# Kernel optimization log

Measured on AMD Instinct MI355X. Metric: run time of the kernel, lower is better.

Reference implementation:

```python
import jax, jax.numpy as jnp
import numpy as np
from jax import lax

VOC = 32000; H = 512; T = 256; B = 64; L = 2; MAXLEN = 32; SOS = 1


def setup_inputs() -> dict:
    key = jax.random.key(0)
    ks = jax.random.split(key, 20)
    s = 1.0 / np.sqrt(H)
    u = lambda k, shape: jax.random.uniform(k, shape, jnp.float32, -s, s)
    inp = {}
    inp["input"] = jax.random.randint(ks[0], (T, B), 0, VOC)
    inp["emb_enc"] = jax.random.normal(ks[1], (VOC, H), jnp.float32) * 0.1
    inp["emb_dec"] = jax.random.normal(ks[2], (VOC, H), jnp.float32) * 0.1
    # GRU weights, torch layout: W_ih (3H, in), W_hh (3H, H), biases (3H,); stacked over layers
    inp["enc_Wih"] = u(ks[3], (L, 3 * H, H)); inp["enc_Whh"] = u(ks[4], (L, 3 * H, H))
    inp["enc_bih"] = u(ks[5], (L, 3 * H));   inp["enc_bhh"] = u(ks[6], (L, 3 * H))
    inp["dec_Wih"] = u(ks[7], (L, 3 * H, H)); inp["dec_Whh"] = u(ks[8], (L, 3 * H, H))
    inp["dec_bih"] = u(ks[9], (L, 3 * H));   inp["dec_bhh"] = u(ks[10], (L, 3 * H))
    inp["attn_W"] = u(ks[11], (T, (L + 1) * H)); inp["attn_b"] = u(ks[12], (T,))
    inp["comb_W"] = u(ks[13], (H, 2 * H));       inp["comb_b"] = u(ks[14], (H,))
    inp["avg_W"] = u(ks[15], (1, H))   # dueling value head, no bias
    inp["adv_W"] = u(ks[16], (VOC, H)) # dueling advantage head, no bias
    return inp


def _gru_cell(x, h, Wih, Whh, bih, bhh):
    gi = x @ Wih.T + bih
    gh = h @ Whh.T + bhh
    ir, iz, in_ = jnp.split(gi, 3, axis=-1)
    hr, hz, hn = jnp.split(gh, 3, axis=-1)
    r = jax.nn.sigmoid(ir + hr)
    z = jax.nn.sigmoid(iz + hz)
    n = jnp.tanh(in_ + r * hn)
    return (1.0 - z) * n + z * h


def _gru_step(x, h, Wih, Whh, bih, bhh):
    # x: (B,H), h: (L,B,H) -> new h (L,B,H), top-layer output (B,H)
    hs = []
    for l in range(L):
        hl = _gru_cell(x, h[l], Wih[l], Whh[l], bih[l], bhh[l])
        hs.append(hl)
        x = hl
    return jnp.stack(hs), x


def _forward(input, emb_enc, emb_dec, enc_Wih, enc_Whh, enc_bih, enc_bhh,
             dec_Wih, dec_Whh, dec_bih, dec_bhh, attn_W, attn_b,
             comb_W, comb_b, avg_W, adv_W):
    # ----- encoder -----
    emb = jax.nn.relu(emb_enc[input])  # (T,B,H)
    h0 = jnp.zeros((L, B, H), jnp.float32)

    def enc_step(h, x):
        h2, top = _gru_step(x, h, enc_Wih, enc_Whh, enc_bih, enc_bhh)
        return h2, top

    states, gru_out = lax.scan(enc_step, h0, emb)  # gru_out: (T,B,H)

    def dec_step(carry, _):
        h, word = carry
        e = jax.nn.relu(emb_dec[word])                       # (B,H)
        sv = jnp.reshape(h, (B, L * H))                      # matches torch .view(-1,1,L*H)
        a = jax.nn.relu(jnp.concatenate([e, sv], -1) @ attn_W.T + attn_b)  # (B,T)
        applied = jnp.einsum('bt,tbh->bh', a, gru_out)       # (B,H)
        comb = jax.nn.relu(jnp.concatenate([e, applied], -1) @ comb_W.T + comb_b)
        h2, top = _gru_step(comb, h, dec_Wih, dec_Whh, dec_bih, dec_bhh)
        values = top @ avg_W.T + top @ adv_W.T               # (B,1)+(B,VOC) -> (B,VOC)
        word2 = jnp.argmax(values, axis=-1)
        q = jnp.take_along_axis(values, word2[:, None], axis=-1)[:, 0]
        return (h2, word2), (top, q)

    word0 = jnp.full((B,), SOS, dtype=jnp.int32)
    _, (tops, qs) = lax.scan(dec_step, (states, word0), None, length=MAXLEN)
    sentences = tops[:, None]  # (MAXLEN,1,B,H) mirrors stacking (1,B,H) rnn_outs
    return sentences, qs       # qs: (MAXLEN,B)


def reference(input, emb_enc, emb_dec, enc_Wih, enc_Whh, enc_bih, enc_bhh,
              dec_Wih, dec_Whh, dec_bih, dec_bhh, attn_W, attn_b,
              comb_W, comb_b, avg_W, adv_W):
    return _forward(input, emb_enc, emb_dec, enc_Wih, enc_Whh, enc_bih, enc_bhh,
                    dec_Wih, dec_Whh, dec_bih, dec_bhh, attn_W, attn_b,
                    comb_W, comb_b, avg_W, adv_W)
```

## Files before the change

### kernel.cpp

```cpp
#include <hip/hip_runtime.h>
#include <math.h>

#define VOCN 32000
#define HN 512
#define TN 256
#define BN 64
#define MAXLENN 32
#define SOSW 1

#define WS_FLAG     0
#define WS_REL      8192
#define WS_H        8448
#define WS_CELLS    (WS_H + 131072)
#define WS_AVG      (WS_CELLS + 4096)
#define WS_A        (WS_AVG + 64)
#define WS_APPLIED  (WS_A + 16384)
#define WS_COMB     (WS_APPLIED + 32768)
#define WS_GRUOUT   (WS_COMB + 32768)
#define WS_ZERO_BYTES ((WS_CELLS + 4096) * 4)

typedef float f4 __attribute__((ext_vector_type(4)));

__device__ __forceinline__ f4 ld4(const float* p) { return *(const f4*)p; }
__device__ __forceinline__ f4 ldnt4(const float* p) {
  return __builtin_nontemporal_load((const f4*)p);
}
__device__ __forceinline__ float dot4(f4 a, f4 b, float acc) {
  acc = fmaf(a.x, b.x, acc); acc = fmaf(a.y, b.y, acc);
  acc = fmaf(a.z, b.z, acc); acc = fmaf(a.w, b.w, acc); return acc;
}
__device__ __forceinline__ f4 relu4(f4 v) {
  v.x = fmaxf(v.x, 0.f); v.y = fmaxf(v.y, 0.f);
  v.z = fmaxf(v.z, 0.f); v.w = fmaxf(v.w, 0.f); return v;
}
__device__ __forceinline__ float sigmoidf_(float x) { return 1.f / (1.f + expf(-x)); }

__device__ __forceinline__ float ldcg(const float* p) {
  float v;
  asm volatile("global_load_dword %0, %1, off sc0 sc1\n\ts_waitcnt vmcnt(0)"
               : "=&v"(v) : "v"(p) : "memory");
  return v;
}
__device__ __forceinline__ void stcg(float* p, float v) {
  asm volatile("global_store_dword %0, %1, off sc0 sc1" :: "v"(p), "v"(v) : "memory");
}
__device__ __forceinline__ void ldcg_b4(const float* p0, const float* p1,
                                        const float* p2, const float* p3,
                                        f4& v0, f4& v1, f4& v2, f4& v3) {
  asm volatile(
      "global_load_dwordx4 %0, %4, off sc0 sc1\n\t"
      "global_load_dwordx4 %1, %5, off sc0 sc1\n\t"
      "global_load_dwordx4 %2, %6, off sc0 sc1\n\t"
      "global_load_dwordx4 %3, %7, off sc0 sc1\n\t"
      "s_waitcnt vmcnt(0)"
      : "=&v"(v0), "=&v"(v1), "=&v"(v2), "=&v"(v3)
      : "v"(p0), "v"(p1), "v"(p2), "v"(p3)
      : "memory");
}
__device__ __forceinline__ void ldcg_b8(const float* p0, const float* p1,
    const float* p2, const float* p3, const float* p4, const float* p5,
    const float* p6, const float* p7,
    f4& v0, f4& v1, f4& v2, f4& v3, f4& v4, f4& v5, f4& v6, f4& v7) {
  asm volatile(
      "global_load_dwordx4 %0, %8, off sc0 sc1\n\t"
      "global_load_dwordx4 %1, %9, off sc0 sc1\n\t"
      "global_load_dwordx4 %2, %10, off sc0 sc1\n\t"
      "global_load_dwordx4 %3, %11, off sc0 sc1\n\t"
      "global_load_dwordx4 %4, %12, off sc0 sc1\n\t"
      "global_load_dwordx4 %5, %13, off sc0 sc1\n\t"
      "global_load_dwordx4 %6, %14, off sc0 sc1\n\t"
      "global_load_dwordx4 %7, %15, off sc0 sc1\n\t"
      "s_waitcnt vmcnt(0)"
      : "=&v"(v0), "=&v"(v1), "=&v"(v2), "=&v"(v3),
        "=&v"(v4), "=&v"(v5), "=&v"(v6), "=&v"(v7)
      : "v"(p0), "v"(p1), "v"(p2), "v"(p3), "v"(p4), "v"(p5), "v"(p6), "v"(p7)
      : "memory");
}
__device__ __forceinline__ void ldcg_row8(const float* p, f4 (&v)[8]) {
  asm volatile(
      "global_load_dwordx4 %0, %8, off sc0 sc1\n\t"
      "global_load_dwordx4 %1, %8, off offset:16 sc0 sc1\n\t"
      "global_load_dwordx4 %2, %8, off offset:32 sc0 sc1\n\t"
      "global_load_dwordx4 %3, %8, off offset:48 sc0 sc1\n\t"
      "global_load_dwordx4 %4, %8, off offset:64 sc0 sc1\n\t"
      "global_load_dwordx4 %5, %8, off offset:80 sc0 sc1\n\t"
      "global_load_dwordx4 %6, %8, off offset:96 sc0 sc1\n\t"
      "global_load_dwordx4 %7, %8, off offset:112 sc0 sc1\n\t"
      "s_waitcnt vmcnt(0)"
      : "=&v"(v[0]), "=&v"(v[1]), "=&v"(v[2]), "=&v"(v[3]),
        "=&v"(v[4]), "=&v"(v[5]), "=&v"(v[6]), "=&v"(v[7])
      : "v"(p)
      : "memory");
}

__device__ __forceinline__ void grid_barrier(int* wsi, int gen) {
  asm volatile("s_waitcnt vmcnt(0) lgkmcnt(0)" ::: "memory");
  __syncthreads();
  const int bid = blockIdx.x;
  const int tid = threadIdx.x;
  if (bid == 0) {
    if (tid == 0)
      __hip_atomic_store(wsi + WS_FLAG, gen, __ATOMIC_RELAXED, __HIP_MEMORY_SCOPE_AGENT);
    int* fp = wsi + WS_FLAG + (tid & 255) * 32;
    for (;;) {
      int v = gen;
      if (tid < 256)
        v = __hip_atomic_load(fp, __ATOMIC_RELAXED, __HIP_MEMORY_SCOPE_AGENT);
      if (__syncthreads_and(v >= gen)) break;
      __builtin_amdgcn_s_sleep(2);
    }
    if (tid < 8)
      __hip_atomic_store(wsi + WS_REL + tid * 16, gen, __ATOMIC_RELAXED, __HIP_MEMORY_SCOPE_AGENT);
    __syncthreads();
  } else {
    if (tid == 0) {
      __hip_atomic_store(wsi + WS_FLAG + bid * 32, gen, __ATOMIC_RELAXED, __HIP_MEMORY_SCOPE_AGENT);
      int* rp = wsi + WS_REL + (bid & 7) * 16;
      while (__hip_atomic_load(rp, __ATOMIC_RELAXED, __HIP_MEMORY_SCOPE_AGENT) < gen)
        __builtin_amdgcn_s_sleep(2);
    }
    __syncthreads();
  }
}

__device__ __forceinline__ unsigned ord_enc(float v) {
  unsigned u = __float_as_uint(v);
  return (u & 0x80000000u) ? ~u : (u | 0x80000000u);
}
__device__ __forceinline__ float ord_dec(unsigned k32) {
  unsigned u = (k32 & 0x80000000u) ? (k32 ^ 0x80000000u) : ~k32;
  return __uint_as_float(u);
}
__device__ __forceinline__ int decode_word(const unsigned long long* cell) {
  unsigned long long key = __hip_atomic_load(cell, __ATOMIC_RELAXED,
                                             __HIP_MEMORY_SCOPE_AGENT);
  int wb = (int)(0xFFFFFFFFu - (unsigned)(key & 0xFFFFFFFFull));
  return wb < 0 ? 0 : (wb > VOCN - 1 ? VOCN - 1 : wb);
}

__device__ __forceinline__ void gru_phase(
    const float* __restrict__ x_base, const int* __restrict__ tok,
    const float* __restrict__ h_rows,
    const float* __restrict__ Wih, const float* __restrict__ Whh,
    const float* __restrict__ bih, const float* __restrict__ bhh,
    float* __restrict__ h_out, float* __restrict__ aux_out,
    int jg, float* lds)
{
  const int tid = threadIdx.x;
  const int tid2 = tid & 255;
  const int bg = tid >> 8;
  f4* x4l = (f4*)lds + (bg << 11);
  f4* h4l = x4l + 1024;

  const float* xp[4]; const float* hp[4]; int loff[4];
#pragma unroll
  for (int i = 0; i < 4; ++i) {
    int tau = tid2 + (i << 8);
    int b = tau >> 5;
    int kq = tau & 31;
    int gb = bg * 32 + b;
    const float* xr = tok ? (x_base + (size_t)tok[gb] * HN) : (x_base + (size_t)gb * HN);
    xp[i] = xr + (kq << 2);
    hp[i] = h_rows + (size_t)gb * HN + (kq << 2);
    loff[i] = (b << 5) + (kq ^ (b & 7));
  }
  const bool cachedx = (tok != nullptr);
  f4 pxv[4], phv[4];
  if (cachedx) {
#pragma unroll
    for (int i = 0; i < 4; ++i) pxv[i] = ld4(xp[i]);
    ldcg_b4(hp[0], hp[1], hp[2], hp[3], phv[0], phv[1], phv[2], phv[3]);
  } else {
    ldcg_b8(xp[0], xp[1], xp[2], xp[3], hp[0], hp[1], hp[2], hp[3],
            pxv[0], pxv[1], pxv[2], pxv[3], phv[0], phv[1], phv[2], phv[3]);
  }

  const int bl = tid2 & 31;
  const int jl = tid2 >> 5;
  const int j = (jg << 3) + jl;
  const float* wi0 = Wih + (size_t)j * HN;
  const float* wi1 = Wih + (size_t)(512 + j) * HN;
  const float* wi2 = Wih + (size_t)(1024 + j) * HN;
  const float* wh0 = Whh + (size_t)j * HN;
  const float* wh1 = Whh + (size_t)(512 + j) * HN;
  const float* wh2 = Whh + (size_t)(1024 + j) * HN;
  float ax0 = 0.f, ax1 = 0.f, ax2 = 0.f, ah0 = 0.f, ah1 = 0.f, ah2 = 0.f;
  const int rdbase = bl << 5;
  const int rdx = bl & 7;

#pragma unroll 1
  for (int ch = 0; ch < 4; ++ch) {
    __syncthreads();
#pragma unroll
    for (int i = 0; i < 4; ++i) {
      x4l[loff[i]] = cachedx ? relu4(pxv[i]) : pxv[i];
      h4l[loff[i]] = phv[i];
    }
    __syncthreads();
    if (ch < 3) {
      const int off = (ch + 1) * 128;
      if (cachedx) {
#pragma unroll
        for (int i = 0; i < 4; ++i) pxv[i] = ld4(xp[i] + off);
        ldcg_b4(hp[0] + off, hp[1] + off, hp[2] + off, hp[3] + off,
                phv[0], phv[1], phv[2], phv[3]);
      } else {
        ldcg_b8(xp[0] + off, xp[1] + off, xp[2] + off, xp[3] + off,
                hp[0] + off, hp[1] + off, hp[2] + off, hp[3] + off,
                pxv[0], pxv[1], pxv[2], pxv[3], phv[0], phv[1], phv[2], phv[3]);
      }
    }
    const int k0 = ch << 7;
#pragma unroll 4
    for (int kq = 0; kq < 32; ++kq) {
      f4 xv = x4l[rdbase + (kq ^ rdx)];
      f4 hv = h4l[rdbase + (kq ^ rdx)];
      const int kk = k0 + (kq << 2);
      ax0 = dot4(xv, ld4(wi0 + kk), ax0);
      ah0 = dot4(hv, ld4(wh0 + kk), ah0);
      ax1 = dot4(xv, ld4(wi1 + kk), ax1);
      ah1 = dot4(hv, ld4(wh1 + kk), ah1);
      ax2 = dot4(xv, ld4(wi2 + kk), ax2);
      ah2 = dot4(hv, ld4(wh2 + kk), ah2);
    }
  }
  const int gb = bg * 32 + bl;
  const float hold = ldcg(h_rows + (size_t)gb * HN + j);
  const float r = sigmoidf_(ax0 + bih[j] + ah0 + bhh[j]);
  const float z = sigmoidf_(ax1 + bih[512 + j] + ah1 + bhh[512 + j]);
  const float n = tanhf(ax2 + bih[1024 + j] + r * (ah2 + bhh[1024 + j]));
  const float hv = (1.f - z) * n + z * hold;
  stcg(h_out + (size_t)gb * HN + j, hv);
  if (aux_out) stcg(aux_out + (size_t)gb * HN + j, hv);
}

__device__ __forceinline__ void d1_attn(
    const float* __restrict__ emb_dec, const unsigned long long* __restrict__ cells,
    int s, const float* __restrict__ hflat, const float* __restrict__ attn_W,
    const float* __restrict__ attn_b, float* __restrict__ a_buf,
    const float* __restrict__ avg_buf, float* __restrict__ qs_base,
    int bid, float* lds)
{
  const int tid = threadIdx.x;
  const int b = tid & 63, q = tid >> 6;
  int* wlds = (int*)(lds + 576);
  if (s > 0 && tid < 64)
    wlds[tid] = decode_word(cells + (size_t)(s - 1) * 64 + tid);
  if (s > 0 && bid == 0 && tid < 64) {
    unsigned long long key = __hip_atomic_load(cells + (size_t)(s - 1) * 64 + tid,
                                               __ATOMIC_RELAXED, __HIP_MEMORY_SCOPE_AGENT);
    qs_base[(size_t)(s - 1) * BN + tid] = ord_dec((unsigned)(key >> 32)) + ldcg(avg_buf + tid);
  }
  __syncthreads();
  const int wb = (s == 0) ? SOSW : wlds[b];
  const float* er = emb_dec + (size_t)wb * HN;
  const float* hr = hflat + b * 1024;
  const float* wr = attn_W + (size_t)bid * 1536;
  float acc = 0.f;
  const int kbeg = q * 192, kend = kbeg + 192;
  int k = kbeg;
  const int kc = (kend < 512) ? kend : 512;
  for (; k < kc; k += 4)
    acc = dot4(relu4(ld4(er + k)), ld4(wr + k), acc);
  if (k < 512) k = 512;
  for (; k < kend; k += 32) {
    f4 hv[8]; ldcg_row8(hr + (k - 512), hv);
#pragma unroll
    for (int jq = 0; jq < 8; ++jq)
      acc = dot4(hv[jq], ld4(wr + k + (jq << 2)), acc);
  }
  __syncthreads();
  lds[(b << 3) + q] = acc;
  __syncthreads();
  if (tid < 64) {
    float v = 0.f;
#pragma unroll
    for (int i = 0; i < 8; ++i) v += lds[(tid << 3) + i];
    v += attn_b[bid];
    stcg(a_buf + tid * 256 + bid, fmaxf(v, 0.f));
  }
}

__device__ __forceinline__ void d2_applied(const float* __restrict__ a_buf,
    const float* __restrict__ gru_out, float* __restrict__ applied, int bid, float* lds)
{
  const int tid = threadIdx.x;
  const int b = bid & 63, hc = bid >> 6;
  f4* al4 = (f4*)lds;
  float* al = lds;
  float* red = lds + 256;
  if (tid < 64) {
    f4 av;
    const float* p = a_buf + b * 256 + (tid << 2);
    asm volatile("global_load_dwordx4 %0, %1, off sc0 sc1\n\ts_waitcnt vmcnt(0)"
                 : "=&v"(av) : "v"(p) : "memory");
    al4[tid] = av;
  }
  __syncthreads();
  const int hl = tid & 127, th = tid >> 7;
  const int hh = (hc << 7) + hl;
  const float* gp = gru_out + (size_t)b * HN + hh;
  float a0 = 0.f, a1 = 0.f, a2 = 0.f, a3 = 0.f;
  float a4 = 0.f, a5 = 0.f, a6 = 0.f, a7 = 0.f;
  const int t0 = th << 6;
#pragma unroll 2
  for (int t = t0; t < t0 + 64; t += 8) {
    a0 = fmaf(al[t + 0], gp[(size_t)(t + 0) * (BN * HN)], a0);
    a1 = fmaf(al[t + 1], gp[(size_t)(t + 1) * (BN * HN)], a1);
    a2 = fmaf(al[t + 2], gp[(size_t)(t + 2) * (BN * HN)], a2);
    a3 = fmaf(al[t + 3], gp[(size_t)(t + 3) * (BN * HN)], a3);
    a4 = fmaf(al[t + 4], gp[(size_t)(t + 4) * (BN * HN)], a4);
    a5 = fmaf(al[t + 5], gp[(size_t)(t + 5) * (BN * HN)], a5);
    a6 = fmaf(al[t + 6], gp[(size_t)(t + 6) * (BN * HN)], a6);
    a7 = fmaf(al[t + 7], gp[(size_t)(t + 7) * (BN * HN)], a7);
  }
  red[tid] = ((a0 + a1) + (a2 + a3)) + ((a4 + a5) + (a6 + a7));
  __syncthreads();
  if (tid < 128)
    stcg(applied + (size_t)b * HN + (hc << 7) + tid,
         red[tid] + red[tid + 128] + red[tid + 256] + red[tid + 384]);
}

__device__ __forceinline__ void d3_comb(const float* __restrict__ emb_dec,
    const unsigned long long* __restrict__ cells, int s,
    const float* __restrict__ applied, const float* __restrict__ comb_W,
    const float* __restrict__ comb_b, float* __restrict__ comb, int bid, float* lds)
{
  const int tid = threadIdx.x;
  const int b = tid & 63, q = tid >> 6;
  int* wlds = (int*)(lds + 1088);
  if (s > 0 && tid < 64)
    wlds[tid] = decode_word(cells + (size_t)(s - 1) * 64 + tid);
  __syncthreads();
  const int wb = (s == 0) ? SOSW : wlds[b];
  const float* er = emb_dec + (size_t)wb * HN;
  const float* apr = applied + (size_t)b * HN;
  const int col0 = bid << 1;
  const float* w0 = comb_W + (size_t)col0 * 1024;
  const float* w1 = w0 + 1024;
  float a0 = 0.f, a1 = 0.f;
  const int kb = q << 7;
  if (q < 4) {
    for (int k = kb; k < kb + 128; k += 4) {
      f4 e = relu4(ld4(er + k));
      a0 = dot4(e, ld4(w0 + k), a0);
      a1 = dot4(e, ld4(w1 + k), a1);
    }
  } else {
#pragma unroll 1
    for (int r = 0; r < 4; ++r) {
      f4 av[8]; ldcg_row8(apr + (kb - 512) + (r << 5), av);
#pragma unroll
      for (int jq = 0; jq < 8; ++jq) {
        a0 = dot4(av[jq], ld4(w0 + kb + (r << 5) + (jq << 2)), a0);
        a1 = dot4(av[jq], ld4(w1 + kb + (r << 5) + (jq << 2)), a1);
      }
    }
  }
  __syncthreads();
  lds[(b << 3) + q] = a0;
  lds[512 + (b << 3) + q] = a1;
  __syncthreads();
  if (tid < 128) {
    const int cc = tid >> 6, b2 = tid & 63;
    const float* base = lds + cc * 512;
    float v = 0.f;
#pragma unroll
    for (int i = 0; i < 8; ++i) v += base[(b2 << 3) + i];
    v += comb_b[col0 + cc];
    stcg(comb + (size_t)b2 * HN + col0 + cc, fmaxf(v, 0.f));
  }
}

__device__ __forceinline__ void d6_values(const float* __restrict__ top,
    const float* __restrict__ adv_W, const float* __restrict__ avg_W,
    unsigned long long* __restrict__ cellsS, float* __restrict__ avg_buf,
    int bid, float* lds)
{
  const int tid = threadIdx.x;
  const int c0 = bid * 125;
  f4* tl = (f4*)lds;
  f4* wl = ((f4*)lds) + 2048;

  const float* tp[4]; int loff[4];
#pragma unroll
  for (int i = 0; i < 4; ++i) {
    int tau = tid + (i << 9);
    int b = tau >> 5, kq = tau & 31;
    tp[i] = top + b * HN + (kq << 2);
    loff[i] = (b << 5) + (kq ^ (b & 7));
  }
  f4 pv[4];
  ldcg_b4(tp[0], tp[1], tp[2], tp[3], pv[0], pv[1], pv[2], pv[3]);

  const int kql = tid & 15;
  const int clb = tid >> 4;
  int cadr[4]; int wdst[4];
#pragma unroll
  for (int r = 0; r < 4; ++r) {
    const int cl = clb + (r << 5);
    int c = c0 + cl; if (c > VOCN - 1) c = VOCN - 1;
    cadr[r] = c;
    wdst[r] = (cl << 4) + (kql ^ ((cl >> 3) & 7));
  }
  f4 wv[4];
#pragma unroll
  for (int r = 0; r < 4; ++r)
    wv[r] = ldnt4(adv_W + (size_t)cadr[r] * HN + (kql << 2));

  const int rp = tid >> 4;
  const int co = tid & 15;
  const int r0 = rp << 1;
  float acc0[8], acc1[8];
#pragma unroll
  for (int i = 0; i < 8; ++i) { acc0[i] = 0.f; acc1[i] = 0.f; }
  float avgacc = 0.f;

#pragma unroll 1
  for (int ph = 0; ph < 8; ++ph) {
    const int ch = ph >> 1, w = ph & 1;
    __syncthreads();
    if (w == 0) {
#pragma unroll
      for (int i = 0; i < 4; ++i) tl[loff[i]] = pv[i];
    }
#pragma unroll
    for (int r = 0; r < 4; ++r) wl[wdst[r]] = wv[r];
    __syncthreads();
    if (ph < 7) {
      const int chn = (ph + 1) >> 1, wn = (ph + 1) & 1;
      const int koff = (chn << 7) + (wn << 6) + (kql << 2);
#pragma unroll
      for (int r = 0; r < 4; ++r)
        wv[r] = ldnt4(adv_W + (size_t)cadr[r] * HN + koff);
    }
    if (w == 0 && ch < 3) {
      const int off = (ch + 1) * 128;
      ldcg_b4(tp[0] + off, tp[1] + off, tp[2] + off, tp[3] + off,
              pv[0], pv[1], pv[2], pv[3]);
    }
    if (w == 0 && bid == 0 && tid < 64) {
#pragma unroll 4
      for (int kq = 0; kq < 32; ++kq)
        avgacc = dot4(tl[(tid << 5) + (kq ^ (tid & 7))],
                      ld4(avg_W + (ch << 7) + (kq << 2)), avgacc);
    }
    const int kqb = w << 4;
#pragma unroll 2
    for (int kqi = 0; kqi < 16; ++kqi) {
      const int kq = kqb + kqi;
      f4 t0v = tl[(r0 << 5) + (kq ^ (r0 & 7))];
      f4 t1v = tl[((r0 + 1) << 5) + (kq ^ ((r0 + 1) & 7))];
#pragma unroll
      for (int j = 0; j < 8; ++j) {
        const int cl = (co << 3) + j;
        f4 wv4 = wl[(cl << 4) + (kqi ^ ((cl >> 3) & 7))];
        acc0[j] = dot4(t0v, wv4, acc0[j]);
        acc1[j] = dot4(t1v, wv4, acc1[j]);
      }
    }
  }
  __syncthreads();

  float bv0 = -3.4e38f, bv1 = -3.4e38f; int bi0 = 2147483647, bi1 = 2147483647;
#pragma unroll
  for (int j = 0; j < 8; ++j) {
    const int cl = (co << 3) + j;
    if (cl < 125) {
      if (acc0[j] > bv0) { bv0 = acc0[j]; bi0 = c0 + cl; }
      if (acc1[j] > bv1) { bv1 = acc1[j]; bi1 = c0 + cl; }
    }
  }
  float* sval = lds;
  int* sidx = (int*)(lds + 1024);
  sval[(r0 << 4) + co] = bv0;  sidx[(r0 << 4) + co] = bi0;
  sval[((r0 + 1) << 4) + co] = bv1;  sidx[((r0 + 1) << 4) + co] = bi1;
  __syncthreads();
  if (tid < 64) {
    float v = sval[tid << 4]; int ii = sidx[tid << 4];
#pragma unroll
    for (int h2 = 1; h2 < 16; ++h2) {
      float v2 = sval[(tid << 4) + h2]; int i2 = sidx[(tid << 4) + h2];
      if (v2 > v || (v2 == v && i2 < ii)) { v = v2; ii = i2; }
    }
    unsigned long long key = ((unsigned long long)ord_enc(v) << 32) |
                             (unsigned long long)(0xFFFFFFFFu - (unsigned)ii);
    __hip_atomic_fetch_max(cellsS + tid, key, __ATOMIC_RELAXED,
                           __HIP_MEMORY_SCOPE_AGENT);
  }
  if (bid == 0 && tid < 64) stcg(avg_buf + tid, avgacc);
}

__global__ void __launch_bounds__(512)
seq2seq_kernel(const int* __restrict__ input, const float* __restrict__ emb_enc,
               const float* __restrict__ emb_dec,
               const float* __restrict__ enc_Wih, const float* __restrict__ enc_Whh,
               const float* __restrict__ enc_bih, const float* __restrict__ enc_bhh,
               const float* __restrict__ dec_Wih, const float* __restrict__ dec_Whh,
               const float* __restrict__ dec_bih, const float* __restrict__ dec_bhh,
               const float* __restrict__ attn_W, const float* __restrict__ attn_b,
               const float* __restrict__ comb_W, const float* __restrict__ comb_b,
               const float* __restrict__ avg_W, const float* __restrict__ adv_W,
               float* __restrict__ out, float* __restrict__ ws)
{
  __shared__ float lds[16384];
  const int bid = blockIdx.x;
  int* wsi = (int*)ws;
  float* hbuf = ws + WS_H;
  unsigned long long* cells = (unsigned long long*)(ws + WS_CELLS);
  float* avg_buf = ws + WS_AVG;
  float* a_buf = ws + WS_A;
  float* applied = ws + WS_APPLIED;
  float* comb = ws + WS_COMB;
  float* gru_out = ws + WS_GRUOUT;
  float* qs_base = out + (size_t)MAXLENN * BN * HN;
  int gen = 0;

#pragma unroll 1
  for (int p = 0; p <= 256; ++p) {
    if (bid < 64) {
      if (p < 256) {
        gru_phase(emb_enc, input + p * BN,
                  hbuf + (size_t)(p & 1) * 65536,
                  enc_Wih, enc_Whh, enc_bih, enc_bhh,
                  hbuf + (size_t)((p + 1) & 1) * 65536,
                  nullptr, bid, lds);
      }
    } else if (bid < 128) {
      if (p >= 1) {
        const int t = p - 1;
        gru_phase(hbuf + (size_t)((t + 1) & 1) * 65536, nullptr,
                  hbuf + (size_t)(t & 1) * 65536 + 32768,
                  enc_Wih + 786432, enc_Whh + 786432,
                  enc_bih + 1536, enc_bhh + 1536,
                  hbuf + (size_t)((t + 1) & 1) * 65536 + 32768,
                  gru_out + (size_t)t * (BN * HN), bid - 64, lds);
      }
    }
    grid_barrier(wsi, ++gen);
  }

  __threadfence();

#pragma unroll 1
  for (int s = 0; s < 32; ++s) {
    const float* hflat = hbuf + (size_t)(s & 1) * 65536;
    float* hnew = hbuf + (size_t)((s + 1) & 1) * 65536;

    d1_attn(emb_dec, cells, s, hflat, attn_W, attn_b, a_buf, avg_buf, qs_base, bid, lds);
    grid_barrier(wsi, ++gen);

    d2_applied(a_buf, gru_out, applied, bid, lds);
    grid_barrier(wsi, ++gen);

    d3_comb(emb_dec, cells, s, applied, comb_W, comb_b, comb, bid, lds);
    grid_barrier(wsi, ++gen);

    if (bid < 64)
      gru_phase(comb, nullptr, hflat, dec_Wih, dec_Whh, dec_bih, dec_bhh,
                hnew, nullptr, bid, lds);
    grid_barrier(wsi, ++gen);

    if (bid < 64)
      gru_phase(hnew, nullptr, hflat + 32768,
                dec_Wih + 786432, dec_Whh + 786432, dec_bih + 1536, dec_bhh + 1536,
                hnew + 32768, out + (size_t)s * (BN * HN), bid, lds);
    grid_barrier(wsi, ++gen);

    d6_values(hnew + 32768, adv_W, avg_W, cells + (size_t)s * 64, avg_buf, bid, lds);
    grid_barrier(wsi, ++gen);
  }

  if (bid == 0 && threadIdx.x < 64) {
    const int tid = threadIdx.x;
    unsigned long long key = __hip_atomic_load(cells + (size_t)31 * 64 + tid,
                                               __ATOMIC_RELAXED, __HIP_MEMORY_SCOPE_AGENT);
    qs_base[(size_t)31 * BN + tid] = ord_dec((unsigned)(key >> 32)) + ldcg(avg_buf + tid);
  }
}

extern "C" void kernel_launch(void* const* d_in, const int* in_sizes, int n_in,
                              void* d_out, int out_size, void* d_ws, size_t ws_size,
                              hipStream_t stream) {
  (void)in_sizes; (void)n_in; (void)out_size; (void)ws_size;
  const int* input      = (const int*)d_in[0];
  const float* emb_enc  = (const float*)d_in[1];
  const float* emb_dec  = (const float*)d_in[2];
  const float* enc_Wih  = (const float*)d_in[3];
  const float* enc_Whh  = (const float*)d_in[4];
  const float* enc_bih  = (const float*)d_in[5];
  const float* enc_bhh  = (const float*)d_in[6];
  const float* dec_Wih  = (const float*)d_in[7];
  const float* dec_Whh  = (const float*)d_in[8];
  const float* dec_bih  = (const float*)d_in[9];
  const float* dec_bhh  = (const float*)d_in[10];
  const float* attn_W   = (const float*)d_in[11];
  const float* attn_b   = (const float*)d_in[12];
  const float* comb_W   = (const float*)d_in[13];
  const float* comb_b   = (const float*)d_in[14];
  const float* avg_W    = (const float*)d_in[15];
  const float* adv_W    = (const float*)d_in[16];
  float* out = (float*)d_out;
  float* ws  = (float*)d_ws;

  hipMemsetAsync(d_ws, 0, WS_ZERO_BYTES, stream);

  seq2seq_kernel<<<dim3(256), dim3(512), 0, stream>>>(
      input, emb_enc, emb_dec, enc_Wih, enc_Whh, enc_bih, enc_bhh,
      dec_Wih, dec_Whh, dec_bih, dec_bhh, attn_W, attn_b,
      comb_W, comb_b, avg_W, adv_W, out, ws);
}
```

Measured before the change: 21.54 ms.

## Retile GRU, attention and combine phases across blocks for better weight reuse

The GRU phase now gives each block 16 hidden units over 32 batch rows instead of 8 units over all 64 rows, so each block stages half the batch activations in LDS. Attention and combine are retiled so each block handles a group of 4 batch rows by 16 attention positions or 32 output columns. The block first stages the concatenated embedding/hidden (or embedding/applied) vectors in LDS, then reads weights with vectorized loads. This is meant to cut redundant per-thread coherent global loads of h and applied and to balance work across blocks. The cost is that weight rows are now read by more blocks.

```diff
diff --git a/kernel.cpp b/kernel.cpp
--- a/kernel.cpp
+++ b/kernel.cpp
@@ -43,6 +43,20 @@
 }
 __device__ __forceinline__ void stcg(float* p, float v) {
   asm volatile("global_store_dword %0, %1, off sc0 sc1" :: "v"(p), "v"(v) : "memory");
+}
+__device__ __forceinline__ void ldcg1(const float* p, f4& v) {
+  asm volatile("global_load_dwordx4 %0, %1, off sc0 sc1\n\ts_waitcnt vmcnt(0)"
+               : "=&v"(v) : "v"(p) : "memory");
+}
+__device__ __forceinline__ void ldcg_b2(const float* p0, const float* p1,
+                                        f4& v0, f4& v1) {
+  asm volatile(
+      "global_load_dwordx4 %0, %2, off sc0 sc1\n\t"
+      "global_load_dwordx4 %1, %3, off sc0 sc1\n\t"
+      "s_waitcnt vmcnt(0)"
+      : "=&v"(v0), "=&v"(v1)
+      : "v"(p0), "v"(p1)
+      : "memory");
 }
 __device__ __forceinline__ void ldcg_b4(const float* p0, const float* p1,
                                         const float* p2, const float* p3,
@@ -57,41 +71,6 @@
       : "v"(p0), "v"(p1), "v"(p2), "v"(p3)
       : "memory");
 }
-__device__ __forceinline__ void ldcg_b8(const float* p0, const float* p1,
-    const float* p2, const float* p3, const float* p4, const float* p5,
-    const float* p6, const float* p7,
-    f4& v0, f4& v1, f4& v2, f4& v3, f4& v4, f4& v5, f4& v6, f4& v7) {
-  asm volatile(
-      "global_load_dwordx4 %0, %8, off sc0 sc1\n\t"
-      "global_load_dwordx4 %1, %9, off sc0 sc1\n\t"
-      "global_load_dwordx4 %2, %10, off sc0 sc1\n\t"
-      "global_load_dwordx4 %3, %11, off sc0 sc1\n\t"
-      "global_load_dwordx4 %4, %12, off sc0 sc1\n\t"
-      "global_load_dwordx4 %5, %13, off sc0 sc1\n\t"
-      "global_load_dwordx4 %6, %14, off sc0 sc1\n\t"
-      "global_load_dwordx4 %7, %15, off sc0 sc1\n\t"
-      "s_waitcnt vmcnt(0)"
-      : "=&v"(v0), "=&v"(v1), "=&v"(v2), "=&v"(v3),
-        "=&v"(v4), "=&v"(v5), "=&v"(v6), "=&v"(v7)
-      : "v"(p0), "v"(p1), "v"(p2), "v"(p3), "v"(p4), "v"(p5), "v"(p6), "v"(p7)
-      : "memory");
-}
-__device__ __forceinline__ void ldcg_row8(const float* p, f4 (&v)[8]) {
-  asm volatile(
-      "global_load_dwordx4 %0, %8, off sc0 sc1\n\t"
-      "global_load_dwordx4 %1, %8, off offset:16 sc0 sc1\n\t"
-      "global_load_dwordx4 %2, %8, off offset:32 sc0 sc1\n\t"
-      "global_load_dwordx4 %3, %8, off offset:48 sc0 sc1\n\t"
-      "global_load_dwordx4 %4, %8, off offset:64 sc0 sc1\n\t"
-      "global_load_dwordx4 %5, %8, off offset:80 sc0 sc1\n\t"
-      "global_load_dwordx4 %6, %8, off offset:96 sc0 sc1\n\t"
-      "global_load_dwordx4 %7, %8, off offset:112 sc0 sc1\n\t"
-      "s_waitcnt vmcnt(0)"
-      : "=&v"(v[0]), "=&v"(v[1]), "=&v"(v[2]), "=&v"(v[3]),
-        "=&v"(v[4]), "=&v"(v[5]), "=&v"(v[6]), "=&v"(v[7])
-      : "v"(p)
-      : "memory");
-}
 
 __device__ __forceinline__ void grid_barrier(int* wsi, int gen) {
   asm volatile("s_waitcnt vmcnt(0) lgkmcnt(0)" ::: "memory");
@@ -144,40 +123,36 @@
     const float* __restrict__ Wih, const float* __restrict__ Whh,
     const float* __restrict__ bih, const float* __restrict__ bhh,
     float* __restrict__ h_out, float* __restrict__ aux_out,
-    int jg, float* lds)
+    int jg, int hg, float* lds)
 {
   const int tid = threadIdx.x;
-  const int tid2 = tid & 255;
-  const int bg = tid >> 8;
-  f4* x4l = (f4*)lds + (bg << 11);
-  f4* h4l = x4l + 1024;
-
-  const float* xp[4]; const float* hp[4]; int loff[4];
-#pragma unroll
-  for (int i = 0; i < 4; ++i) {
-    int tau = tid2 + (i << 8);
-    int b = tau >> 5;
-    int kq = tau & 31;
-    int gb = bg * 32 + b;
+  f4* x4l = (f4*)lds;
+  f4* h4l = ((f4*)lds) + 1024;
+
+  const float* xp[2]; const float* hp[2]; int loff[2];
+#pragma unroll
+  for (int i = 0; i < 2; ++i) {
+    int qq = tid + (i << 9);
+    int b = qq >> 5;
+    int kq = qq & 31;
+    int gb = hg * 32 + b;
     const float* xr = tok ? (x_base + (size_t)tok[gb] * HN) : (x_base + (size_t)gb * HN);
     xp[i] = xr + (kq << 2);
     hp[i] = h_rows + (size_t)gb * HN + (kq << 2);
     loff[i] = (b << 5) + (kq ^ (b & 7));
   }
   const bool cachedx = (tok != nullptr);
-  f4 pxv[4], phv[4];
+  f4 pxv[2], phv[2];
   if (cachedx) {
-#pragma unroll
-    for (int i = 0; i < 4; ++i) pxv[i] = ld4(xp[i]);
-    ldcg_b4(hp[0], hp[1], hp[2], hp[3], phv[0], phv[1], phv[2], phv[3]);
+    pxv[0] = ld4(xp[0]); pxv[1] = ld4(xp[1]);
+    ldcg_b2(hp[0], hp[1], phv[0], phv[1]);
   } else {
-    ldcg_b8(xp[0], xp[1], xp[2], xp[3], hp[0], hp[1], hp[2], hp[3],
-            pxv[0], pxv[1], pxv[2], pxv[3], phv[0], phv[1], phv[2], phv[3]);
-  }
-
-  const int bl = tid2 & 31;
-  const int jl = tid2 >> 5;
-  const int j = (jg << 3) + jl;
+    ldcg_b4(xp[0], xp[1], hp[0], hp[1], pxv[0], pxv[1], phv[0], phv[1]);
+  }
+
+  const int bl = tid & 31;
+  const int jl = tid >> 5;
+  const int j = jg * 16 + jl;
   const float* wi0 = Wih + (size_t)j * HN;
   const float* wi1 = Wih + (size_t)(512 + j) * HN;
   const float* wi2 = Wih + (size_t)(1024 + j) * HN;
@@ -192,7 +167,7 @@
   for (int ch = 0; ch < 4; ++ch) {
     __syncthreads();
 #pragma unroll
-    for (int i = 0; i < 4; ++i) {
+    for (int i = 0; i < 2; ++i) {
       x4l[loff[i]] = cachedx ? relu4(pxv[i]) : pxv[i];
       h4l[loff[i]] = phv[i];
     }
@@ -200,14 +175,11 @@
     if (ch < 3) {
       const int off = (ch + 1) * 128;
       if (cachedx) {
-#pragma unroll
-        for (int i = 0; i < 4; ++i) pxv[i] = ld4(xp[i] + off);
-        ldcg_b4(hp[0] + off, hp[1] + off, hp[2] + off, hp[3] + off,
-                phv[0], phv[1], phv[2], phv[3]);
+        pxv[0] = ld4(xp[0] + off); pxv[1] = ld4(xp[1] + off);
+        ldcg_b2(hp[0] + off, hp[1] + off, phv[0], phv[1]);
       } else {
-        ldcg_b8(xp[0] + off, xp[1] + off, xp[2] + off, xp[3] + off,
-                hp[0] + off, hp[1] + off, hp[2] + off, hp[3] + off,
-                pxv[0], pxv[1], pxv[2], pxv[3], phv[0], phv[1], phv[2], phv[3]);
+        ldcg_b4(xp[0] + off, xp[1] + off, hp[0] + off, hp[1] + off,
+                pxv[0], pxv[1], phv[0], phv[1]);
       }
     }
     const int k0 = ch << 7;
@@ -224,7 +196,7 @@
       ah2 = dot4(hv, ld4(wh2 + kk), ah2);
     }
   }
-  const int gb = bg * 32 + bl;
+  const int gb = hg * 32 + bl;
   const float hold = ldcg(h_rows + (size_t)gb * HN + j);
   const float r = sigmoidf_(ax0 + bih[j] + ah0 + bhh[j]);
   const float z = sigmoidf_(ax1 + bih[512 + j] + ah1 + bhh[512 + j]);
@@ -242,42 +214,52 @@
     int bid, float* lds)
 {
   const int tid = threadIdx.x;
-  const int b = tid & 63, q = tid >> 6;
-  int* wlds = (int*)(lds + 576);
-  if (s > 0 && tid < 64)
-    wlds[tid] = decode_word(cells + (size_t)(s - 1) * 64 + tid);
+  const int bg = bid >> 4, tg = bid & 15;
+  f4* catq = (f4*)lds;
+  float* redl = lds + 6144;
+  int* wlds = (int*)(lds + 6656);
+  if (tid < 4)
+    wlds[tid] = (s == 0) ? SOSW
+              : decode_word(cells + (size_t)(s - 1) * 64 + bg * 4 + tid);
   if (s > 0 && bid == 0 && tid < 64) {
     unsigned long long key = __hip_atomic_load(cells + (size_t)(s - 1) * 64 + tid,
                                                __ATOMIC_RELAXED, __HIP_MEMORY_SCOPE_AGENT);
     qs_base[(size_t)(s - 1) * BN + tid] = ord_dec((unsigned)(key >> 32)) + ldcg(avg_buf + tid);
   }
   __syncthreads();
-  const int wb = (s == 0) ? SOSW : wlds[b];
-  const float* er = emb_dec + (size_t)wb * HN;
-  const float* hr = hflat + b * 1024;
-  const float* wr = attn_W + (size_t)bid * 1536;
+  {
+    const int b0 = tid >> 8, r0q = tid & 255;
+    const int b1 = b0 + 2,   r1q = r0q;
+    f4 h0, h1;
+    ldcg_b2(hflat + (size_t)(bg * 4 + b0) * 1024 + (r0q << 2),
+            hflat + (size_t)(bg * 4 + b1) * 1024 + (r1q << 2), h0, h1);
+    catq[b0 * 384 + 128 + r0q] = h0;
+    catq[b1 * 384 + 128 + r1q] = h1;
+  }
+  {
+    const int b = tid >> 7, kq = tid & 127;
+    const float* er = emb_dec + (size_t)wlds[b] * HN;
+    catq[b * 384 + kq] = relu4(ld4(er + (kq << 2)));
+  }
+  __syncthreads();
+  const int o = tid & 63, seg = tid >> 6;
+  const int bi = o >> 4, ti = o & 15;
+  const int t = tg * 16 + ti;
+  const float* wr = attn_W + (size_t)t * 1536 + seg * 192;
+  const f4* cb = catq + bi * 384 + seg * 48;
   float acc = 0.f;
-  const int kbeg = q * 192, kend = kbeg + 192;
-  int k = kbeg;
-  const int kc = (kend < 512) ? kend : 512;
-  for (; k < kc; k += 4)
-    acc = dot4(relu4(ld4(er + k)), ld4(wr + k), acc);
-  if (k < 512) k = 512;
-  for (; k < kend; k += 32) {
-    f4 hv[8]; ldcg_row8(hr + (k - 512), hv);
-#pragma unroll
-    for (int jq = 0; jq < 8; ++jq)
-      acc = dot4(hv[jq], ld4(wr + k + (jq << 2)), acc);
-  }
-  __syncthreads();
-  lds[(b << 3) + q] = acc;
+#pragma unroll 8
+  for (int qi = 0; qi < 48; ++qi)
+    acc = dot4(cb[qi], ld4(wr + (qi << 2)), acc);
+  redl[o * 8 + seg] = acc;
   __syncthreads();
   if (tid < 64) {
     float v = 0.f;
 #pragma unroll
-    for (int i = 0; i < 8; ++i) v += lds[(tid << 3) + i];
-    v += attn_b[bid];
-    stcg(a_buf + tid * 256 + bid, fmaxf(v, 0.f));
+    for (int i = 0; i < 8; ++i) v += redl[tid * 8 + i];
+    const int b = bg * 4 + (tid >> 4), t2 = tg * 16 + (tid & 15);
+    v += attn_b[t2];
+    stcg(a_buf + b * 256 + t2, fmaxf(v, 0.f));
   }
 }
 
@@ -327,48 +309,41 @@
     const float* __restrict__ comb_b, float* __restrict__ comb, int bid, float* lds)
 {
   const int tid = threadIdx.x;
-  const int b = tid & 63, q = tid >> 6;
-  int* wlds = (int*)(lds + 1088);
-  if (s > 0 && tid < 64)
-    wlds[tid] = decode_word(cells + (size_t)(s - 1) * 64 + tid);
-  __syncthreads();
-  const int wb = (s == 0) ? SOSW : wlds[b];
-  const float* er = emb_dec + (size_t)wb * HN;
-  const float* apr = applied + (size_t)b * HN;
-  const int col0 = bid << 1;
-  const float* w0 = comb_W + (size_t)col0 * 1024;
-  const float* w1 = w0 + 1024;
-  float a0 = 0.f, a1 = 0.f;
-  const int kb = q << 7;
-  if (q < 4) {
-    for (int k = kb; k < kb + 128; k += 4) {
-      f4 e = relu4(ld4(er + k));
-      a0 = dot4(e, ld4(w0 + k), a0);
-      a1 = dot4(e, ld4(w1 + k), a1);
-    }
-  } else {
-#pragma unroll 1
-    for (int r = 0; r < 4; ++r) {
-      f4 av[8]; ldcg_row8(apr + (kb - 512) + (r << 5), av);
-#pragma unroll
-      for (int jq = 0; jq < 8; ++jq) {
-        a0 = dot4(av[jq], ld4(w0 + kb + (r << 5) + (jq << 2)), a0);
-        a1 = dot4(av[jq], ld4(w1 + kb + (r << 5) + (jq << 2)), a1);
-      }
-    }
-  }
-  __syncthreads();
-  lds[(b << 3) + q] = a0;
-  lds[512 + (b << 3) + q] = a1;
+  const int bg = bid & 15, cg = bid >> 4;
+  f4* cat2q = (f4*)lds;
+  float* red2 = lds + 4096;
+  int* wlds = (int*)(lds + 4608);
+  if (tid < 4)
+    wlds[tid] = (s == 0) ? SOSW
+              : decode_word(cells + (size_t)(s - 1) * 64 + bg * 4 + tid);
+  __syncthreads();
+  {
+    const int b = tid >> 7, kq = tid & 127;
+    f4 av;
+    ldcg1(applied + (size_t)(bg * 4 + b) * HN + (kq << 2), av);
+    cat2q[b * 256 + 128 + kq] = av;
+  }
+  {
+    const int b = tid >> 7, kq = tid & 127;
+    cat2q[b * 256 + kq] = relu4(ld4(emb_dec + (size_t)wlds[b] * HN + (kq << 2)));
+  }
+  __syncthreads();
+  const int o = tid & 127, seg = tid >> 7;
+  const int bi = o >> 5, cj = o & 31;
+  const int col = cg * 32 + cj;
+  const float* wr = comb_W + (size_t)col * 1024 + seg * 256;
+  const f4* cb = cat2q + bi * 256 + seg * 64;
+  float acc = 0.f;
+#pragma unroll 8
+  for (int qi = 0; qi < 64; ++qi)
+    acc = dot4(cb[qi], ld4(wr + (qi << 2)), acc);
+  red2[o * 4 + seg] = acc;
   __syncthreads();
   if (tid < 128) {
-    const int cc = tid >> 6, b2 = tid & 63;
-    const float* base = lds + cc * 512;
-    float v = 0.f;
-#pragma unroll
-    for (int i = 0; i < 8; ++i) v += base[(b2 << 3) + i];
-    v += comb_b[col0 + cc];
-    stcg(comb + (size_t)b2 * HN + col0 + cc, fmaxf(v, 0.f));
+    const int b = bg * 4 + (tid >> 5), c2 = cg * 32 + (tid & 31);
+    float v = red2[tid * 4] + red2[tid * 4 + 1] + red2[tid * 4 + 2] + red2[tid * 4 + 3];
+    v += comb_b[c2];
+    stcg(comb + (size_t)b * HN + c2, fmaxf(v, 0.f));
   }
 }
 
@@ -524,17 +499,18 @@
                   hbuf + (size_t)(p & 1) * 65536,
                   enc_Wih, enc_Whh, enc_bih, enc_bhh,
                   hbuf + (size_t)((p + 1) & 1) * 65536,
-                  nullptr, bid, lds);
+                  nullptr, bid >> 1, bid & 1, lds);
       }
     } else if (bid < 128) {
       if (p >= 1) {
         const int t = p - 1;
+        const int rb = bid - 64;
         gru_phase(hbuf + (size_t)((t + 1) & 1) * 65536, nullptr,
                   hbuf + (size_t)(t & 1) * 65536 + 32768,
                   enc_Wih + 786432, enc_Whh + 786432,
                   enc_bih + 1536, enc_bhh + 1536,
                   hbuf + (size_t)((t + 1) & 1) * 65536 + 32768,
-                  gru_out + (size_t)t * (BN * HN), bid - 64, lds);
+                  gru_out + (size_t)t * (BN * HN), rb >> 1, rb & 1, lds);
       }
     }
     grid_barrier(wsi, ++gen);
@@ -558,13 +534,13 @@
 
     if (bid < 64)
       gru_phase(comb, nullptr, hflat, dec_Wih, dec_Whh, dec_bih, dec_bhh,
-                hnew, nullptr, bid, lds);
+                hnew, nullptr, bid >> 1, bid & 1, lds);
     grid_barrier(wsi, ++gen);
 
     if (bid < 64)
       gru_phase(hnew, nullptr, hflat + 32768,
                 dec_Wih + 786432, dec_Whh + 786432, dec_bih + 1536, dec_bhh + 1536,
-                hnew + 32768, out + (size_t)s * (BN * HN), bid, lds);
+                hnew + 32768, out + (size_t)s * (BN * HN), bid >> 1, bid & 1, lds);
     grid_barrier(wsi, ++gen);
 
     d6_values(hnew + 32768, adv_W, avg_W, cells + (size_t)s * 64, avg_buf, bid, lds);
```

Measured after the change: 20.82 ms. -3.4%, faster.
